# Kernel optimization log

Measured on AMD Instinct MI355X. Metric: run time of the kernel, lower is better.

## Reference

```python
import jax, jax.numpy as jnp
import numpy as np

N = 100000   # nodes
E = 800000   # edges
H = 256      # hidden_dim == input_dim
L = 3        # num_layers
G = 64       # graphs in batch


def setup_inputs() -> dict:
    key = jax.random.key(0)
    ks = jax.random.split(key, 16)
    s = 0.05
    inp = {
        'x': jax.random.normal(ks[0], (N, H), jnp.float32),
        'edge_index': jax.random.randint(ks[1], (2, E), 0, N, dtype=jnp.int32),
        'batch': jnp.sort(jax.random.randint(ks[2], (N,), 0, G, dtype=jnp.int32)),
        'Ws': jax.random.normal(ks[3], (L, H, H), jnp.float32) * s,
        'Wn': jax.random.normal(ks[4], (L, H, H), jnp.float32) * s,
        'bs': jnp.zeros((L, H), jnp.float32),
        'att_w': jax.random.normal(ks[5], (H, 1), jnp.float32) * s,
        'att_b': jnp.zeros((1,), jnp.float32),
        'ne_W1': jax.random.normal(ks[6], (H, H // 2), jnp.float32) * s,
        'ne_b1': jnp.zeros((H // 2,), jnp.float32),
        'ne_W2': jax.random.normal(ks[7], (H // 2, 1), jnp.float32) * s,
        'ne_b2': jnp.zeros((1,), jnp.float32),
        'nd_W1': jax.random.normal(ks[8], (H, H // 2), jnp.float32) * s,
        'nd_b1': jnp.zeros((H // 2,), jnp.float32),
        'nd_W2': jax.random.normal(ks[9], (H // 2, 1), jnp.float32) * s,
        'nd_b2': jnp.zeros((1,), jnp.float32),
    }
    return inp


def reference(x, edge_index, batch, Ws, Wn, bs, att_w, att_b,
              ne_W1, ne_b1, ne_W2, ne_b2, nd_W1, nd_b1, nd_W2, nd_b2):
    src, dst = edge_index[0], edge_index[1]
    n = x.shape[0]
    # in-degree for mean aggregation (clamped to avoid div-by-zero)
    deg = jax.ops.segment_sum(jnp.ones(src.shape[0], x.dtype), dst, num_segments=n)
    deg = jnp.maximum(deg, 1.0)[:, None]                    # [N,1]
    # GNN encoder: SAGE-mean layers, ReLU (dropout identity at eval)
    h = x
    for l in range(Ws.shape[0]):
        msg = jax.ops.segment_sum(h[src], dst, num_segments=n) / deg  # [N,H]
        h = jax.nn.relu(h @ Ws[l] + msg @ Wn[l] + bs[l])
    # attention pooling: per-graph softmax over node scores
    s = (h @ att_w + att_b)[:, 0]                           # [N]
    m = jax.ops.segment_max(s, batch, num_segments=G)
    e = jnp.exp(s - m[batch])
    denom = jax.ops.segment_sum(e, batch, num_segments=G)
    alpha = (e / denom[batch])[:, None]                     # [N,1]
    g = jax.ops.segment_sum(alpha * h, batch, num_segments=G)  # [G,H]
    # heads: Linear-ReLU-(Dropout)-Linear
    graph_logits = jax.nn.relu(g @ ne_W1 + ne_b1) @ ne_W2 + ne_b2  # [G,1]
    node_logits = jax.nn.relu(h @ nd_W1 + nd_b1) @ nd_W2 + nd_b2  # [N,1]
    return (graph_logits, node_logits)
```

## Files before the change

### kernel.cpp

```cpp
#include <hip/hip_runtime.h>
#include <hip/hip_bf16.h>

#define HID 256
#define HHALF 128
#define LSTR 40

typedef unsigned short u16;
typedef __attribute__((ext_vector_type(8))) short bf16x8;
typedef __attribute__((ext_vector_type(4))) float f32x4;

__device__ __forceinline__ float bf2f(unsigned int u) {
    unsigned int x = (u & 0xffffu) << 16;
    union { unsigned int i; float f; } c; c.i = x; return c.f;
}
__device__ __forceinline__ u16 f2bf(float f) {
    __hip_bfloat16 h = __float2bfloat16(f);
    union { __hip_bfloat16 h; u16 u; } c; c.h = h; return c.u;
}

__global__ void k_count(const int* __restrict__ dst, int* __restrict__ cnt, int E) {
    int i = blockIdx.x * blockDim.x + threadIdx.x;
    if (i < E) atomicAdd(&cnt[dst[i]], 1);
}

__global__ void k_scan_block(const int* __restrict__ cnt, int* __restrict__ bsum, int n) {
    __shared__ int sd[256];
    int tid = threadIdx.x;
    int i = blockIdx.x * 256 + tid;
    int v = (i < n) ? cnt[i] : 0;
    sd[tid] = v; __syncthreads();
    for (int s = 128; s > 0; s >>= 1) {
        if (tid < s) sd[tid] += sd[tid + s];
        __syncthreads();
    }
    if (tid == 0) bsum[blockIdx.x] = sd[0];
}

__global__ void k_scan_top(int* __restrict__ bsum, int nb) {
    __shared__ int sd[512];
    int t = threadIdx.x;
    int v = (t < nb) ? bsum[t] : 0;
    sd[t] = v; __syncthreads();
    for (int s = 1; s < 512; s <<= 1) {
        int x = (t >= s) ? sd[t - s] : 0;
        __syncthreads();
        sd[t] += x;
        __syncthreads();
    }
    if (t < nb) bsum[t] = sd[t] - v;
}

__global__ void k_scan_down(const int* __restrict__ cnt, const int* __restrict__ boff,
                            int* __restrict__ row_off, int n, int total) {
    __shared__ int sd[256];
    int tid = threadIdx.x;
    int i = blockIdx.x * 256 + tid;
    int v = (i < n) ? cnt[i] : 0;
    sd[tid] = v; __syncthreads();
    for (int s = 1; s < 256; s <<= 1) {
        int x = (tid >= s) ? sd[tid - s] : 0;
        __syncthreads();
        sd[tid] += x;
        __syncthreads();
    }
    if (i < n) row_off[i] = boff[blockIdx.x] + sd[tid] - v;
    if (i == 0) row_off[n] = total;
}

__global__ void k_scatter(const int* __restrict__ src, const int* __restrict__ dst,
                          const int* __restrict__ row_off, int* __restrict__ fill,
                          int* __restrict__ col, int E) {
    int i = blockIdx.x * blockDim.x + threadIdx.x;
    if (i < E) {
        int d = dst[i];
        int p = atomicAdd(&fill[d], 1);
        col[row_off[d] + p] = src[i];
    }
}

__global__ void k_f2b(const float* __restrict__ in, u16* __restrict__ o, int total4) {
    int i = blockIdx.x * blockDim.x + threadIdx.x;
    if (i >= total4) return;
    float4 v = *(const float4*)&in[(size_t)i * 4];
    uint2 p;
    p.x = (unsigned)f2bf(v.x) | ((unsigned)f2bf(v.y) << 16);
    p.y = (unsigned)f2bf(v.z) | ((unsigned)f2bf(v.w) << 16);
    *(uint2*)&o[(size_t)i * 4] = p;
}

__global__ void k_wt(const float* __restrict__ W, u16* __restrict__ Wt, int K, int C) {
    int idx = blockIdx.x * blockDim.x + threadIdx.x;
    if (idx >= K * C) return;
    int k = idx / C, c = idx - k * C;
    Wt[c * K + k] = f2bf(W[idx]);
}

__global__ __launch_bounds__(256) void k_agg(
    const u16* __restrict__ h, const int* __restrict__ row_off,
    const int* __restrict__ col, u16* __restrict__ msg, int n) {
    int node = blockIdx.x * 4 + (threadIdx.x >> 6);
    if (node >= n) return;
    int t = threadIdx.x & 63;
    int s0 = row_off[node], s1 = row_off[node + 1];
    float a0 = 0.f, a1 = 0.f, a2 = 0.f, a3 = 0.f;
    int e = s0;
    for (; e + 4 <= s1; e += 4) {
        int c0 = col[e], c1 = col[e + 1], c2 = col[e + 2], c3 = col[e + 3];
        uint2 v0 = *(const uint2*)&h[(size_t)c0 * HID + t * 4];
        uint2 v1 = *(const uint2*)&h[(size_t)c1 * HID + t * 4];
        uint2 v2 = *(const uint2*)&h[(size_t)c2 * HID + t * 4];
        uint2 v3 = *(const uint2*)&h[(size_t)c3 * HID + t * 4];
        a0 += bf2f(v0.x) + bf2f(v1.x) + bf2f(v2.x) + bf2f(v3.x);
        a1 += bf2f(v0.x >> 16) + bf2f(v1.x >> 16) + bf2f(v2.x >> 16) + bf2f(v3.x >> 16);
        a2 += bf2f(v0.y) + bf2f(v1.y) + bf2f(v2.y) + bf2f(v3.y);
        a3 += bf2f(v0.y >> 16) + bf2f(v1.y >> 16) + bf2f(v2.y >> 16) + bf2f(v3.y >> 16);
    }
    for (; e < s1; ++e) {
        int c = col[e];
        uint2 v = *(const uint2*)&h[(size_t)c * HID + t * 4];
        a0 += bf2f(v.x); a1 += bf2f(v.x >> 16);
        a2 += bf2f(v.y); a3 += bf2f(v.y >> 16);
    }
    int deg = s1 - s0;
    float inv = 1.0f / (float)(deg > 1 ? deg : 1);
    uint2 o;
    o.x = (unsigned)f2bf(a0 * inv) | ((unsigned)f2bf(a1 * inv) << 16);
    o.y = (unsigned)f2bf(a2 * inv) | ((unsigned)f2bf(a3 * inv) << 16);
    *(uint2*)&msg[(size_t)node * HID + t * 4] = o;
}

__global__ __launch_bounds__(512) void k_gemm_bf(
    const u16* __restrict__ A1, const u16* __restrict__ W1t,
    const u16* __restrict__ A2, const u16* __restrict__ W2t,
    const float* __restrict__ bias, u16* __restrict__ out,
    int n, int ncols) {
    __shared__ __align__(16) u16 As[128 * LSTR];
    __shared__ __align__(16) u16 Bs[256 * LSTR];
    const int tid  = threadIdx.x;
    const int lane = tid & 63;
    const int w    = tid >> 6;
    const int wr   = w >> 2, wc = w & 3;
    const int brow = blockIdx.x * 128;
    const int nkt  = A2 ? 16 : 8;

    f32x4 acc[4][4];
    #pragma unroll
    for (int m = 0; m < 4; ++m)
        #pragma unroll
        for (int q = 0; q < 4; ++q)
            acc[m][q] = (f32x4){0.f, 0.f, 0.f, 0.f};

    const int sr  = tid >> 2;
    const int sck = (tid & 3) * 8;
    int arow = brow + sr; if (arow >= n) arow = n - 1;
    const size_t abase  = (size_t)arow * HID + sck;
    const size_t b0base = (size_t)sr * HID + sck;
    const size_t b1base = (size_t)(sr + 128) * HID + sck;

    const int lr = lane & 15;
    const int kc = (lane >> 4) * 8;

    for (int kt = 0; kt < nkt; ++kt) {
        const u16* A = (kt < 8) ? A1 : A2;
        const u16* W = (kt < 8) ? W1t : W2t;
        const int k0 = (kt & 7) * 32;
        uint4 av  = *(const uint4*)(A + abase + k0);
        uint4 bv0 = *(const uint4*)(W + b0base + k0);
        uint4 bv1 = *(const uint4*)(W + b1base + k0);
        __syncthreads();
        *(uint4*)&As[sr * LSTR + sck] = av;
        *(uint4*)&Bs[sr * LSTR + sck] = bv0;
        *(uint4*)&Bs[(sr + 128) * LSTR + sck] = bv1;
        __syncthreads();
        bf16x8 af[4], bg[4];
        #pragma unroll
        for (int m = 0; m < 4; ++m)
            af[m] = *(const bf16x8*)&As[(wr * 64 + m * 16 + lr) * LSTR + kc];
        #pragma unroll
        for (int q = 0; q < 4; ++q)
            bg[q] = *(const bf16x8*)&Bs[(wc * 64 + q * 16 + lr) * LSTR + kc];
        #pragma unroll
        for (int m = 0; m < 4; ++m)
            #pragma unroll
            for (int q = 0; q < 4; ++q)
                acc[m][q] = __builtin_amdgcn_mfma_f32_16x16x32_bf16(
                    bg[q], af[m], acc[m][q], 0, 0, 0);
    }

    const int lq = lane >> 4;
    #pragma unroll
    for (int m = 0; m < 4; ++m) {
        int row = brow + wr * 64 + m * 16 + lr;
        if (row >= n) continue;
        #pragma unroll
        for (int q = 0; q < 4; ++q) {
            int col = wc * 64 + q * 16 + lq * 4;
            if (col < ncols) {
                float4 bb = *(const float4*)&bias[col];
                uint2 o;
                o.x = (unsigned)f2bf(fmaxf(acc[m][q][0] + bb.x, 0.f))
                    | ((unsigned)f2bf(fmaxf(acc[m][q][1] + bb.y, 0.f)) << 16);
                o.y = (unsigned)f2bf(fmaxf(acc[m][q][2] + bb.z, 0.f))
                    | ((unsigned)f2bf(fmaxf(acc[m][q][3] + bb.w, 0.f)) << 16);
                *(uint2*)&out[(size_t)row * ncols + col] = o;
            }
        }
    }
}

__global__ void k_score(const u16* __restrict__ h, const float* __restrict__ att_w,
                        const float* __restrict__ att_b, float* __restrict__ s, int n) {
    int gw = (blockIdx.x * blockDim.x + threadIdx.x) >> 6;
    int lane = threadIdx.x & 63;
    if (gw >= n) return;
    uint2 v = *(const uint2*)&h[(size_t)gw * HID + lane * 4];
    float4 wv = *(const float4*)&att_w[lane * 4];
    float p = bf2f(v.x) * wv.x + bf2f(v.x >> 16) * wv.y
            + bf2f(v.y) * wv.z + bf2f(v.y >> 16) * wv.w;
    #pragma unroll
    for (int off = 32; off; off >>= 1) p += __shfl_xor(p, off, 64);
    if (lane == 0) s[gw] = p + att_b[0];
}

__global__ void k_gstart(const int* __restrict__ batch, int* __restrict__ gstart, int n, int G) {
    int i = blockIdx.x * blockDim.x + threadIdx.x;
    if (i >= n) return;
    int b = batch[i];
    int bp = (i == 0) ? -1 : batch[i - 1];
    for (int g = bp + 1; g <= b; ++g) gstart[g] = i;
    if (i == n - 1) {
        for (int g = b + 1; g <= G; ++g) gstart[g] = n;
    }
}

__global__ void k_mdenom(const float* __restrict__ s, const int* __restrict__ gstart,
                         float* __restrict__ m, float* __restrict__ denom) {
    int g = blockIdx.x;
    int t = threadIdx.x;
    int i0 = gstart[g], i1 = gstart[g + 1];
    __shared__ float red[256];
    float mx = -INFINITY;
    for (int i = i0 + t; i < i1; i += 256) mx = fmaxf(mx, s[i]);
    red[t] = mx; __syncthreads();
    for (int st = 128; st; st >>= 1) {
        if (t < st) red[t] = fmaxf(red[t], red[t + st]);
        __syncthreads();
    }
    float gm = red[0];
    __syncthreads();
    float sm = 0.f;
    for (int i = i0 + t; i < i1; i += 256) sm += expf(s[i] - gm);
    red[t] = sm; __syncthreads();
    for (int st = 128; st; st >>= 1) {
        if (t < st) red[t] += red[t + st];
        __syncthreads();
    }
    if (t == 0) { m[g] = gm; denom[g] = red[0]; }
}

__global__ void k_alpha(const float* __restrict__ s, const int* __restrict__ batch,
                        const float* __restrict__ m, const float* __restrict__ denom,
                        float* __restrict__ alpha, int n) {
    int i = blockIdx.x * blockDim.x + threadIdx.x;
    if (i >= n) return;
    int b = batch[i];
    float d = denom[b];
    alpha[i] = (d > 0.f) ? expf(s[i] - m[b]) / d : 0.f;
}

__global__ void k_pool(const u16* __restrict__ h, const float* __restrict__ alpha,
                       const int* __restrict__ gstart, float* __restrict__ gpool) {
    int g = blockIdx.x, sp = blockIdx.y, t = threadIdx.x;
    int i0 = gstart[g], i1 = gstart[g + 1];
    int len = i1 - i0;
    int a = i0 + (int)((long long)len * sp / 16);
    int b = i0 + (int)((long long)len * (sp + 1) / 16);
    float acc = 0.f;
    for (int i = a; i < b; ++i) acc += alpha[i] * bf2f(h[(size_t)i * HID + t]);
    if (acc != 0.f || sp == 0) atomicAdd(&gpool[g * HID + t], acc);
}

__global__ void k_ghead(const float* __restrict__ gpool, const float* __restrict__ W1,
                        const float* __restrict__ b1, const float* __restrict__ W2,
                        const float* __restrict__ b2, float* __restrict__ out) {
    int g = blockIdx.x, t = threadIdx.x;
    __shared__ float row[HID];
    __shared__ float red[128];
    row[t] = gpool[g * HID + t];
    row[t + 128] = gpool[g * HID + t + 128];
    __syncthreads();
    float acc = 0.f;
    #pragma unroll 8
    for (int k = 0; k < HID; ++k) acc = fmaf(row[k], W1[k * HHALF + t], acc);
    float hid = fmaxf(acc + b1[t], 0.f);
    red[t] = hid * W2[t];
    __syncthreads();
    for (int st = 64; st; st >>= 1) {
        if (t < st) red[t] += red[t + st];
        __syncthreads();
    }
    if (t == 0) out[g] = red[0] + b2[0];
}

__global__ void k_ndot(const u16* __restrict__ hid, const float* __restrict__ W2,
                       const float* __restrict__ b2, float* __restrict__ out, int n) {
    int gw = (blockIdx.x * blockDim.x + threadIdx.x) >> 6;
    int lane = threadIdx.x & 63;
    if (gw >= n) return;
    unsigned v = *(const unsigned*)&hid[(size_t)gw * HHALF + lane * 2];
    float val = bf2f(v) * W2[lane * 2] + bf2f(v >> 16) * W2[lane * 2 + 1];
    #pragma unroll
    for (int off = 32; off; off >>= 1) val += __shfl_xor(val, off, 64);
    if (lane == 0) out[gw] = val + b2[0];
}

extern "C" void kernel_launch(void* const* d_in, const int* in_sizes, int n_in,
                              void* d_out, int out_size, void* d_ws, size_t ws_size,
                              hipStream_t stream) {
    const float* x      = (const float*)d_in[0];
    const int*   eidx   = (const int*)d_in[1];
    const int*   batch  = (const int*)d_in[2];
    const float* Ws     = (const float*)d_in[3];
    const float* Wn     = (const float*)d_in[4];
    const float* bs     = (const float*)d_in[5];
    const float* att_w  = (const float*)d_in[6];
    const float* att_b  = (const float*)d_in[7];
    const float* ne_W1  = (const float*)d_in[8];
    const float* ne_b1  = (const float*)d_in[9];
    const float* ne_W2  = (const float*)d_in[10];
    const float* ne_b2  = (const float*)d_in[11];
    const float* nd_W1  = (const float*)d_in[12];
    const float* nd_b1  = (const float*)d_in[13];
    const float* nd_W2  = (const float*)d_in[14];
    const float* nd_b2  = (const float*)d_in[15];
    float* out = (float*)d_out;

    const int N = in_sizes[2];
    const int E = in_sizes[1] / 2;
    const int L = in_sizes[3] / (HID * HID);
    const int G = out_size - N;

    const int* src = eidx;
    const int* dst = eidx + E;

    size_t off = 0;
    auto alloc = [&](size_t bytes) {
        void* p = (char*)d_ws + off;
        off += (bytes + 255) & ~(size_t)255;
        return p;
    };
    int*   cnt     = (int*)alloc((size_t)N * 4);
    int*   row_off = (int*)alloc((size_t)(N + 1) * 4);
    int*   fill    = (int*)alloc((size_t)N * 4);
    int*   col     = (int*)alloc((size_t)E * 4);
    int*   gstart  = (int*)alloc((size_t)(G + 1) * 4);
    int*   bsum    = (int*)alloc(1024 * 4);
    float* sarr    = (float*)alloc((size_t)N * 4);
    float* alpha   = (float*)alloc((size_t)N * 4);
    float* marr    = (float*)alloc((size_t)G * 4);
    float* denom   = (float*)alloc((size_t)G * 4);
    float* gpool   = (float*)alloc((size_t)G * HID * 4);
    u16*   xb      = (u16*)alloc((size_t)N * HID * 2);
    u16*   msgb    = (u16*)alloc((size_t)N * HID * 2);
    u16*   hb1     = (u16*)alloc((size_t)N * HID * 2);
    u16*   hb2     = (u16*)alloc((size_t)N * HID * 2);
    u16*   hidb    = (u16*)alloc((size_t)N * HHALF * 2);
    u16*   WsT     = (u16*)alloc((size_t)L * HID * HID * 2);
    u16*   WnT     = (u16*)alloc((size_t)L * HID * HID * 2);
    u16*   ndW1T   = (u16*)alloc((size_t)HID * HID * 2);
    (void)ws_size;

    const int eb = (E + 255) / 256;
    const int nb = (N + 255) / 256;

    hipMemsetAsync(cnt, 0, (size_t)N * 4, stream);
    k_count<<<eb, 256, 0, stream>>>(dst, cnt, E);
    k_scan_block<<<nb, 256, 0, stream>>>(cnt, bsum, N);
    k_scan_top<<<1, 512, 0, stream>>>(bsum, nb);
    k_scan_down<<<nb, 256, 0, stream>>>(cnt, bsum, row_off, N, E);
    hipMemsetAsync(fill, 0, (size_t)N * 4, stream);
    k_scatter<<<eb, 256, 0, stream>>>(src, dst, row_off, fill, col, E);

    k_f2b<<<(N * HID / 4 + 255) / 256, 256, 0, stream>>>(x, xb, N * HID / 4);
    for (int l = 0; l < L; ++l) {
        k_wt<<<(HID * HID + 255) / 256, 256, 0, stream>>>(
            Ws + (size_t)l * HID * HID, WsT + (size_t)l * HID * HID, HID, HID);
        k_wt<<<(HID * HID + 255) / 256, 256, 0, stream>>>(
            Wn + (size_t)l * HID * HID, WnT + (size_t)l * HID * HID, HID, HID);
    }
    k_wt<<<(HID * HHALF + 255) / 256, 256, 0, stream>>>(nd_W1, ndW1T, HID, HHALF);

    const int gx = (N + 127) / 128;
    const u16* hin = xb;
    u16* hout = hb1;
    for (int l = 0; l < L; ++l) {
        k_agg<<<(N + 3) / 4, 256, 0, stream>>>(hin, row_off, col, msgb, N);
        k_gemm_bf<<<gx, 512, 0, stream>>>(
            hin, WsT + (size_t)l * HID * HID, msgb, WnT + (size_t)l * HID * HID,
            bs + (size_t)l * HID, hout, N, HID);
        hin = hout;
        hout = (hout == hb1) ? hb2 : hb1;
    }
    const u16* h = hin;

    k_score<<<(N + 3) / 4, 256, 0, stream>>>(h, att_w, att_b, sarr, N);
    k_gstart<<<nb, 256, 0, stream>>>(batch, gstart, N, G);
    k_mdenom<<<G, 256, 0, stream>>>(sarr, gstart, marr, denom);
    k_alpha<<<nb, 256, 0, stream>>>(sarr, batch, marr, denom, alpha, N);
    hipMemsetAsync(gpool, 0, (size_t)G * HID * 4, stream);
    k_pool<<<dim3(G, 16), HID, 0, stream>>>(h, alpha, gstart, gpool);

    k_ghead<<<G, HHALF, 0, stream>>>(gpool, ne_W1, ne_b1, ne_W2, ne_b2, out);

    k_gemm_bf<<<gx, 512, 0, stream>>>(
        h, ndW1T, nullptr, nullptr, nd_b1, hidb, N, HHALF);
    k_ndot<<<(N + 3) / 4, 256, 0, stream>>>(hidb, nd_W2, nd_b2, out + G, N);
}
```

Before: 613.9 us.

## Use direct global-to-LDS loads with XOR swizzle, widen aggregation loads, merge weight transposes

The GEMM tile staging now uses global_load_lds, so data goes straight from global memory into unpadded LDS, with an XOR swizzle on the 16-byte chunks to avoid bank conflicts. This removes the register round trip and the padding. The neighbor aggregation now uses 16-byte loads, with each half-wavefront handling alternate edges and a cross-half shuffle reduction at the end. The seven weight-transpose launches are merged into one kernel to cut launch overhead. The risk is that the direct-to-LDS path depends on the lane-to-address layout matching the swizzled reads exactly.

```diff
diff --git a/kernel.cpp b/kernel.cpp
--- a/kernel.cpp
+++ b/kernel.cpp
@@ -3,7 +3,6 @@
 
 #define HID 256
 #define HHALF 128
-#define LSTR 40
 
 typedef unsigned short u16;
 typedef __attribute__((ext_vector_type(8))) short bf16x8;
@@ -13,9 +12,21 @@
     unsigned int x = (u & 0xffffu) << 16;
     union { unsigned int i; float f; } c; c.i = x; return c.f;
 }
+__device__ __forceinline__ float lof(unsigned u) {
+    union { unsigned i; float f; } c; c.i = u << 16; return c.f;
+}
+__device__ __forceinline__ float hif(unsigned u) {
+    union { unsigned i; float f; } c; c.i = u & 0xffff0000u; return c.f;
+}
 __device__ __forceinline__ u16 f2bf(float f) {
     __hip_bfloat16 h = __float2bfloat16(f);
     union { __hip_bfloat16 h; u16 u; } c; c.h = h; return c.u;
+}
+
+__device__ __forceinline__ void gload16(const u16* g, u16* l) {
+    __builtin_amdgcn_global_load_lds(
+        (const __attribute__((address_space(1))) void*)g,
+        (__attribute__((address_space(3))) void*)l, 16, 0, 0);
 }
 
 __global__ void k_count(const int* __restrict__ dst, int* __restrict__ cnt, int E) {
@@ -88,11 +99,22 @@
     *(uint2*)&o[(size_t)i * 4] = p;
 }
 
-__global__ void k_wt(const float* __restrict__ W, u16* __restrict__ Wt, int K, int C) {
-    int idx = blockIdx.x * blockDim.x + threadIdx.x;
-    if (idx >= K * C) return;
-    int k = idx / C, c = idx - k * C;
-    Wt[c * K + k] = f2bf(W[idx]);
+__global__ void k_wt_all(const float* __restrict__ Ws, const float* __restrict__ Wn,
+                         const float* __restrict__ ndW1,
+                         u16* __restrict__ WsT, u16* __restrict__ WnT,
+                         u16* __restrict__ ndW1T, int L) {
+    int idx = blockIdx.x * 256 + threadIdx.x;
+    int mat = idx >> 16;
+    int r = idx & 65535;
+    int k = r >> 8, c = r & 255;
+    if (mat < L) {
+        WsT[(size_t)mat * 65536 + c * 256 + k] = f2bf(Ws[(size_t)mat * 65536 + k * 256 + c]);
+    } else if (mat < 2 * L) {
+        int l = mat - L;
+        WnT[(size_t)l * 65536 + c * 256 + k] = f2bf(Wn[(size_t)l * 65536 + k * 256 + c]);
+    } else {
+        if (c < HHALF) ndW1T[c * 256 + k] = f2bf(ndW1[k * HHALF + c]);
+    }
 }
 
 __global__ __launch_bounds__(256) void k_agg(
@@ -100,33 +122,47 @@
     const int* __restrict__ col, u16* __restrict__ msg, int n) {
     int node = blockIdx.x * 4 + (threadIdx.x >> 6);
     if (node >= n) return;
-    int t = threadIdx.x & 63;
+    int lane = threadIdx.x & 63;
+    int half = lane >> 5;
+    int t = lane & 31;
     int s0 = row_off[node], s1 = row_off[node + 1];
     float a0 = 0.f, a1 = 0.f, a2 = 0.f, a3 = 0.f;
+    float a4 = 0.f, a5 = 0.f, a6 = 0.f, a7 = 0.f;
     int e = s0;
     for (; e + 4 <= s1; e += 4) {
-        int c0 = col[e], c1 = col[e + 1], c2 = col[e + 2], c3 = col[e + 3];
-        uint2 v0 = *(const uint2*)&h[(size_t)c0 * HID + t * 4];
-        uint2 v1 = *(const uint2*)&h[(size_t)c1 * HID + t * 4];
-        uint2 v2 = *(const uint2*)&h[(size_t)c2 * HID + t * 4];
-        uint2 v3 = *(const uint2*)&h[(size_t)c3 * HID + t * 4];
-        a0 += bf2f(v0.x) + bf2f(v1.x) + bf2f(v2.x) + bf2f(v3.x);
-        a1 += bf2f(v0.x >> 16) + bf2f(v1.x >> 16) + bf2f(v2.x >> 16) + bf2f(v3.x >> 16);
-        a2 += bf2f(v0.y) + bf2f(v1.y) + bf2f(v2.y) + bf2f(v3.y);
-        a3 += bf2f(v0.y >> 16) + bf2f(v1.y >> 16) + bf2f(v2.y >> 16) + bf2f(v3.y >> 16);
-    }
-    for (; e < s1; ++e) {
-        int c = col[e];
-        uint2 v = *(const uint2*)&h[(size_t)c * HID + t * 4];
-        a0 += bf2f(v.x); a1 += bf2f(v.x >> 16);
-        a2 += bf2f(v.y); a3 += bf2f(v.y >> 16);
-    }
-    int deg = s1 - s0;
-    float inv = 1.0f / (float)(deg > 1 ? deg : 1);
-    uint2 o;
-    o.x = (unsigned)f2bf(a0 * inv) | ((unsigned)f2bf(a1 * inv) << 16);
-    o.y = (unsigned)f2bf(a2 * inv) | ((unsigned)f2bf(a3 * inv) << 16);
-    *(uint2*)&msg[(size_t)node * HID + t * 4] = o;
+        int c0 = col[e + half];
+        int c1 = col[e + 2 + half];
+        uint4 v0 = *(const uint4*)&h[(size_t)c0 * HID + t * 8];
+        uint4 v1 = *(const uint4*)&h[(size_t)c1 * HID + t * 8];
+        a0 += lof(v0.x) + lof(v1.x); a1 += hif(v0.x) + hif(v1.x);
+        a2 += lof(v0.y) + lof(v1.y); a3 += hif(v0.y) + hif(v1.y);
+        a4 += lof(v0.z) + lof(v1.z); a5 += hif(v0.z) + hif(v1.z);
+        a6 += lof(v0.w) + lof(v1.w); a7 += hif(v0.w) + hif(v1.w);
+    }
+    for (; e < s1; e += 2) {
+        if (e + half < s1) {
+            int c = col[e + half];
+            uint4 v = *(const uint4*)&h[(size_t)c * HID + t * 8];
+            a0 += lof(v.x); a1 += hif(v.x);
+            a2 += lof(v.y); a3 += hif(v.y);
+            a4 += lof(v.z); a5 += hif(v.z);
+            a6 += lof(v.w); a7 += hif(v.w);
+        }
+    }
+    a0 += __shfl_xor(a0, 32); a1 += __shfl_xor(a1, 32);
+    a2 += __shfl_xor(a2, 32); a3 += __shfl_xor(a3, 32);
+    a4 += __shfl_xor(a4, 32); a5 += __shfl_xor(a5, 32);
+    a6 += __shfl_xor(a6, 32); a7 += __shfl_xor(a7, 32);
+    if (half == 0) {
+        int deg = s1 - s0;
+        float inv = 1.0f / (float)(deg > 1 ? deg : 1);
+        uint4 o;
+        o.x = (unsigned)f2bf(a0 * inv) | ((unsigned)f2bf(a1 * inv) << 16);
+        o.y = (unsigned)f2bf(a2 * inv) | ((unsigned)f2bf(a3 * inv) << 16);
+        o.z = (unsigned)f2bf(a4 * inv) | ((unsigned)f2bf(a5 * inv) << 16);
+        o.w = (unsigned)f2bf(a6 * inv) | ((unsigned)f2bf(a7 * inv) << 16);
+        *(uint4*)&msg[(size_t)node * HID + t * 8] = o;
+    }
 }
 
 __global__ __launch_bounds__(512) void k_gemm_bf(
@@ -134,8 +170,8 @@
     const u16* __restrict__ A2, const u16* __restrict__ W2t,
     const float* __restrict__ bias, u16* __restrict__ out,
     int n, int ncols) {
-    __shared__ __align__(16) u16 As[128 * LSTR];
-    __shared__ __align__(16) u16 Bs[256 * LSTR];
+    __shared__ __align__(16) u16 As[128 * 32];
+    __shared__ __align__(16) u16 Bs[256 * 32];
     const int tid  = threadIdx.x;
     const int lane = tid & 63;
     const int w    = tid >> 6;
@@ -150,35 +186,41 @@
         for (int q = 0; q < 4; ++q)
             acc[m][q] = (f32x4){0.f, 0.f, 0.f, 0.f};
 
-    const int sr  = tid >> 2;
-    const int sck = (tid & 3) * 8;
-    int arow = brow + sr; if (arow >= n) arow = n - 1;
-    const size_t abase  = (size_t)arow * HID + sck;
-    const size_t b0base = (size_t)sr * HID + sck;
-    const size_t b1base = (size_t)(sr + 128) * HID + sck;
+    const int arow_t = w * 16 + (lane >> 2);
+    int arow = brow + arow_t; if (arow >= n) arow = n - 1;
+    const int ach = (lane & 3) ^ ((arow_t >> 1) & 3);
+    const size_t abase = (size_t)arow * HID + ach * 8;
+    u16* As_dst = &As[(w * 16) * 32];
+
+    const int brow0 = w * 32 + (lane >> 2);
+    const int bch0  = (lane & 3) ^ ((brow0 >> 1) & 3);
+    const size_t bbase0 = (size_t)brow0 * HID + bch0 * 8;
+    u16* Bs_dst0 = &Bs[(w * 32) * 32];
+    const int brow1 = brow0 + 16;
+    const int bch1  = (lane & 3) ^ ((brow1 >> 1) & 3);
+    const size_t bbase1 = (size_t)brow1 * HID + bch1 * 8;
+    u16* Bs_dst1 = &Bs[(w * 32 + 16) * 32];
 
     const int lr = lane & 15;
-    const int kc = (lane >> 4) * 8;
+    const int lq = lane >> 4;
+    const int ph = lq ^ ((lr >> 1) & 3);
 
     for (int kt = 0; kt < nkt; ++kt) {
         const u16* A = (kt < 8) ? A1 : A2;
         const u16* W = (kt < 8) ? W1t : W2t;
         const int k0 = (kt & 7) * 32;
-        uint4 av  = *(const uint4*)(A + abase + k0);
-        uint4 bv0 = *(const uint4*)(W + b0base + k0);
-        uint4 bv1 = *(const uint4*)(W + b1base + k0);
-        __syncthreads();
-        *(uint4*)&As[sr * LSTR + sck] = av;
-        *(uint4*)&Bs[sr * LSTR + sck] = bv0;
-        *(uint4*)&Bs[(sr + 128) * LSTR + sck] = bv1;
+        __syncthreads();
+        gload16(A + abase + k0, As_dst);
+        gload16(W + bbase0 + k0, Bs_dst0);
+        gload16(W + bbase1 + k0, Bs_dst1);
         __syncthreads();
         bf16x8 af[4], bg[4];
         #pragma unroll
         for (int m = 0; m < 4; ++m)
-            af[m] = *(const bf16x8*)&As[(wr * 64 + m * 16 + lr) * LSTR + kc];
+            af[m] = *(const bf16x8*)&As[(wr * 64 + m * 16 + lr) * 32 + ph * 8];
         #pragma unroll
         for (int q = 0; q < 4; ++q)
-            bg[q] = *(const bf16x8*)&Bs[(wc * 64 + q * 16 + lr) * LSTR + kc];
+            bg[q] = *(const bf16x8*)&Bs[(wc * 64 + q * 16 + lr) * 32 + ph * 8];
         #pragma unroll
         for (int m = 0; m < 4; ++m)
             #pragma unroll
@@ -187,7 +229,6 @@
                     bg[q], af[m], acc[m][q], 0, 0, 0);
     }
 
-    const int lq = lane >> 4;
     #pragma unroll
     for (int m = 0; m < 4; ++m) {
         int row = brow + wr * 64 + m * 16 + lr;
@@ -382,13 +423,8 @@
     k_scatter<<<eb, 256, 0, stream>>>(src, dst, row_off, fill, col, E);
 
     k_f2b<<<(N * HID / 4 + 255) / 256, 256, 0, stream>>>(x, xb, N * HID / 4);
-    for (int l = 0; l < L; ++l) {
-        k_wt<<<(HID * HID + 255) / 256, 256, 0, stream>>>(
-            Ws + (size_t)l * HID * HID, WsT + (size_t)l * HID * HID, HID, HID);
-        k_wt<<<(HID * HID + 255) / 256, 256, 0, stream>>>(
-            Wn + (size_t)l * HID * HID, WnT + (size_t)l * HID * HID, HID, HID);
-    }
-    k_wt<<<(HID * HHALF + 255) / 256, 256, 0, stream>>>(nd_W1, ndW1T, HID, HHALF);
+    k_wt_all<<<(2 * L + 1) * (HID * HID / 256), 256, 0, stream>>>(
+        Ws, Wn, nd_W1, WsT, WnT, ndW1T, L);
 
     const int gx = (N + 127) / 128;
     const u16* hin = xb;
```

Result: faster. 586.4 us (-4.5%).
